# Optimization experiments

Hardware: AMD Instinct MI355X
Metric: run time of the kernel (lower is better)

## Reference

```python
import jax, jax.numpy as jnp
import numpy as np

EPS = 1e-6
BETA = 0.5
B, T, N = 128, 30, 10000   # batch, BP iterations, n error bits
M, K = 5000, 10            # checks, observables
CHK_W, OBS_W = 6, 50       # row weights of chkmat / obsmat


def _make_supports():
    """Deterministic sparse supports (CSR-style flattened col indices + row ids)."""
    rng = np.random.default_rng(0)
    chk_rows = np.argpartition(rng.random((M, N)), CHK_W, axis=1)[:, :CHK_W]
    obs_rows = np.argpartition(rng.random((K, N)), OBS_W, axis=1)[:, :OBS_W]
    chk_idx = chk_rows.reshape(-1).astype(np.int32)
    chk_seg = np.repeat(np.arange(M, dtype=np.int32), CHK_W)
    obs_idx = obs_rows.reshape(-1).astype(np.int32)
    obs_seg = np.repeat(np.arange(K, dtype=np.int32), OBS_W)
    return chk_idx, chk_seg, obs_idx, obs_seg


def setup_inputs() -> dict:
    key = jax.random.key(0)
    k1, k2, k3 = jax.random.split(key, 3)
    all_llrs = jax.random.normal(k1, (B, T, N), dtype=jnp.float32) * 2.0
    syndromes = jax.random.randint(k2, (B, M), 0, 2, dtype=jnp.int32)
    observables = jax.random.randint(k3, (B, K), 0, 2, dtype=jnp.int32)
    chk_idx, chk_seg, obs_idx, obs_seg = _make_supports()
    return {
        "all_llrs": all_llrs,
        "syndromes": syndromes,
        "observables": observables,
        "chk_idx": jnp.asarray(chk_idx),
        "chk_seg": jnp.asarray(chk_seg),
        "obs_idx": jnp.asarray(obs_idx),
        "obs_seg": jnp.asarray(obs_seg),
    }


def _pred_llr(t, idx, seg, num_seg):
    # t: (B,T,N) tanh(llr/2); gather support cols -> (B,T,E)
    g = t[:, :, idx]
    # segmented product over support entries (tanh rule), segments on axis 0
    p = jax.ops.segment_prod(jnp.moveaxis(g, 2, 0), seg, num_segments=num_seg)  # (S,B,T)
    p = jnp.clip(jnp.moveaxis(p, 0, 2), -1.0 + EPS, 1.0 - EPS)  # (B,T,S)
    return 2.0 * jnp.arctanh(p)


def _bce_with_logits(z, y):
    # stable BCEWithLogits: max(z,0) - z*y + log(1+exp(-|z|)) == logaddexp(0,z) - z*y
    return jnp.logaddexp(0.0, z) - z * y


def reference(all_llrs, syndromes, observables, chk_idx, chk_seg, obs_idx, obs_seg):
    t = jnp.tanh(all_llrs * 0.5)                                   # (B,T,N)
    syn_llr = _pred_llr(t, chk_idx, chk_seg, syndromes.shape[1])    # (B,T,M)
    obs_llr = _pred_llr(t, obs_idx, obs_seg, observables.shape[1])  # (B,T,K)
    y_syn = syndromes.astype(jnp.float32)[:, None, :]
    y_obs = observables.astype(jnp.float32)[:, None, :]
    loss1 = _bce_with_logits(-syn_llr, y_syn).sum(axis=2)           # (B,T)
    loss2 = _bce_with_logits(-obs_llr, y_obs).sum(axis=2)           # (B,T)
    loss = BETA * loss1 + (1.0 - BETA) * loss2
    return loss.mean()
```

## Files before the change

### kernel.cpp

```cpp
#include <hip/hip_runtime.h>
#include <hip/hip_bf16.h>

#define B_  128
#define T_  30
#define N_  10000
#define M_  5000
#define K_  10
#define CHK_W_ 6
#define OBS_W_ 50
#define EPS_ 1e-6f
#define LOG2_ 0.69314718056f

__global__ __launch_bounds__(256) void decode_loss_kernel(
    const float* __restrict__ all_llrs,
    const int*   __restrict__ syndromes,
    const int*   __restrict__ observables,
    const int*   __restrict__ chk_idx,
    const int*   __restrict__ obs_idx,
    float*       __restrict__ out)
{
    __shared__ float tn[N_];
    __shared__ float red[4];

    const int bt  = blockIdx.x;
    const int b   = bt / T_;
    const int tid = threadIdx.x;

    const float4* row4 = (const float4*)(all_llrs + (size_t)bt * N_);
    float4* tn4 = (float4*)tn;
    for (int i = tid; i < N_/4; i += 256) {
        float4 v = row4[i];
        float4 r;
        r.x = 1.f - 2.f / (__expf(v.x) + 1.f);
        r.y = 1.f - 2.f / (__expf(v.y) + 1.f);
        r.z = 1.f - 2.f / (__expf(v.z) + 1.f);
        r.w = 1.f - 2.f / (__expf(v.w) + 1.f);
        tn4[i] = r;
    }
    __syncthreads();

    float acc1 = 0.f;
    const int* syn = syndromes + (size_t)b * M_;
    for (int m = tid; m < M_; m += 256) {
        const int* ci = chk_idx + m * CHK_W_;
        float p = tn[ci[0]] * tn[ci[1]] * tn[ci[2]]
                * tn[ci[3]] * tn[ci[4]] * tn[ci[5]];
        p = fminf(fmaxf(p, -1.f + EPS_), 1.f - EPS_);
        float sp = syn[m] ? -p : p;
        acc1 += LOG2_ - __logf(1.f + sp);
    }

    float acc2 = 0.f;
    const int* obs = observables + (size_t)b * K_;
    for (int k = tid; k < K_; k += 256) {
        const int* oi = obs_idx + k * OBS_W_;
        float p = 1.f;
        #pragma unroll 10
        for (int j = 0; j < OBS_W_; ++j) p *= tn[oi[j]];
        p = fminf(fmaxf(p, -1.f + EPS_), 1.f - EPS_);
        float sp = obs[k] ? -p : p;
        acc2 += LOG2_ - __logf(1.f + sp);
    }

    float acc = 0.5f * acc1 + 0.5f * acc2;

    #pragma unroll
    for (int off = 32; off > 0; off >>= 1)
        acc += __shfl_down(acc, off, 64);
    if ((tid & 63) == 0) red[tid >> 6] = acc;
    __syncthreads();
    if (tid == 0) {
        float s = red[0] + red[1] + red[2] + red[3];
        atomicAdd(out, s * (1.f / (B_ * T_)));
    }
}

extern "C" void kernel_launch(void* const* d_in, const int* in_sizes, int n_in,
                              void* d_out, int out_size, void* d_ws, size_t ws_size,
                              hipStream_t stream) {
    const float* all_llrs    = (const float*)d_in[0];
    const int*   syndromes   = (const int*)d_in[1];
    const int*   observables = (const int*)d_in[2];
    const int*   chk_idx     = (const int*)d_in[3];
    const int*   obs_idx     = (const int*)d_in[5];
    float* out = (float*)d_out;

    hipMemsetAsync(out, 0, sizeof(float) * out_size, stream);

    dim3 grid(B_ * T_);
    dim3 block(256);
    decode_loss_kernel<<<grid, block, 0, stream>>>(
        all_llrs, syndromes, observables, chk_idx, obs_idx, out);
}
```

Baseline: 287.2 us.

## Split into tanh-transpose to fp16 column-major, then coalesced gather-loss kernel

A first kernel computes tanh and writes the result transposed to an (N, B*T) half-precision workspace. A second kernel has each lane handle two (b,t) rows as a half2 and gathers check and observable columns with coalesced loads, splitting checks into chunks across a 2D grid. This replaces the per-row LDS staging and scattered shared-memory gathers, but adds an extra pass through global memory and lowers the product to fp16 precision. Products of 50 fp16 terms may lose accuracy or underflow.

```diff
diff --git a/kernel.cpp b/kernel.cpp
--- a/kernel.cpp
+++ b/kernel.cpp
@@ -1,5 +1,5 @@
 #include <hip/hip_runtime.h>
-#include <hip/hip_bf16.h>
+#include <hip/hip_fp16.h>
 
 #define B_  128
 #define T_  30
@@ -9,69 +9,117 @@
 #define CHK_W_ 6
 #define OBS_W_ 50
 #define EPS_ 1e-6f
-#define LOG2_ 0.69314718056f
+#define LOG2F_ 0.69314718056f
+#define BT_ (B_*T_)
+#define RG_ 128
+#define NGRP_ (BT_/RG_)
+#define CHUNK_ 100
+#define NCHK_BLK_ (M_/CHUNK_)
 
-__global__ __launch_bounds__(256) void decode_loss_kernel(
-    const float* __restrict__ all_llrs,
-    const int*   __restrict__ syndromes,
-    const int*   __restrict__ observables,
-    const int*   __restrict__ chk_idx,
-    const int*   __restrict__ obs_idx,
-    float*       __restrict__ out)
+__global__ __launch_bounds__(256) void tanh_transpose_kernel(
+    const float* __restrict__ llrs,
+    __half*      __restrict__ tt)
 {
-    __shared__ float tn[N_];
-    __shared__ float red[4];
+    __shared__ float tile[64][65];
+    const int bt0 = blockIdx.x * 64;
+    const int n0  = blockIdx.y * 64;
+    const int tid = threadIdx.x;
+    const int c   = tid & 63;
+    const int r4  = tid >> 6;
 
-    const int bt  = blockIdx.x;
-    const int b   = bt / T_;
-    const int tid = threadIdx.x;
-
-    const float4* row4 = (const float4*)(all_llrs + (size_t)bt * N_);
-    float4* tn4 = (float4*)tn;
-    for (int i = tid; i < N_/4; i += 256) {
-        float4 v = row4[i];
-        float4 r;
-        r.x = 1.f - 2.f / (__expf(v.x) + 1.f);
-        r.y = 1.f - 2.f / (__expf(v.y) + 1.f);
-        r.z = 1.f - 2.f / (__expf(v.z) + 1.f);
-        r.w = 1.f - 2.f / (__expf(v.w) + 1.f);
-        tn4[i] = r;
+    if (n0 + c < N_) {
+        #pragma unroll
+        for (int i = 0; i < 16; ++i) {
+            int r = i * 4 + r4;
+            float v = llrs[(size_t)(bt0 + r) * N_ + (n0 + c)];
+            tile[r][c] = 1.f - 2.f / (__expf(v) + 1.f);
+        }
     }
     __syncthreads();
 
-    float acc1 = 0.f;
-    const int* syn = syndromes + (size_t)b * M_;
-    for (int m = tid; m < M_; m += 256) {
-        const int* ci = chk_idx + m * CHK_W_;
-        float p = tn[ci[0]] * tn[ci[1]] * tn[ci[2]]
-                * tn[ci[3]] * tn[ci[4]] * tn[ci[5]];
-        p = fminf(fmaxf(p, -1.f + EPS_), 1.f - EPS_);
-        float sp = syn[m] ? -p : p;
-        acc1 += LOG2_ - __logf(1.f + sp);
+    const int r = tid & 63;
+    #pragma unroll
+    for (int i = 0; i < 16; ++i) {
+        int cc = i * 4 + r4;
+        if (n0 + cc < N_)
+            tt[(size_t)(n0 + cc) * BT_ + (bt0 + r)] = __float2half(tile[r][cc]);
+    }
+}
+
+__global__ __launch_bounds__(256) void gather_loss_kernel(
+    const __half* __restrict__ tt,
+    const int*    __restrict__ syndromes,
+    const int*    __restrict__ observables,
+    const int*    __restrict__ chk_idx,
+    const int*    __restrict__ obs_idx,
+    float*        __restrict__ out)
+{
+    const int tid  = threadIdx.x;
+    const int lane = tid & 63;
+    const int wave = tid >> 6;
+    const int bt0  = blockIdx.x * RG_;
+    const int r0   = bt0 + 2 * lane;
+    const int b0   = r0 / T_;
+    const int b1   = (r0 + 1) / T_;
+    const __half2* tt2 = (const __half2*)tt;
+    const int half_off = r0 >> 1;
+
+    float acc = 0.f;
+    const int y = blockIdx.y;
+
+    if (y < NCHK_BLK_) {
+        const int* syn0 = syndromes + (size_t)b0 * M_;
+        const int* syn1 = syndromes + (size_t)b1 * M_;
+        const int m0 = y * CHUNK_ + wave * (CHUNK_ / 4);
+        #pragma unroll 2
+        for (int m = m0; m < m0 + CHUNK_ / 4; ++m) {
+            const int* ci = chk_idx + m * CHK_W_;
+            __half2 a0 = tt2[(size_t)ci[0] * (BT_/2) + half_off];
+            __half2 a1 = tt2[(size_t)ci[1] * (BT_/2) + half_off];
+            __half2 a2 = tt2[(size_t)ci[2] * (BT_/2) + half_off];
+            __half2 a3 = tt2[(size_t)ci[3] * (BT_/2) + half_off];
+            __half2 a4 = tt2[(size_t)ci[4] * (BT_/2) + half_off];
+            __half2 a5 = tt2[(size_t)ci[5] * (BT_/2) + half_off];
+            __half2 q  = __hmul2(__hmul2(__hmul2(a0, a1), __hmul2(a2, a3)),
+                                 __hmul2(a4, a5));
+            float p0 = __low2float(q);
+            float p1 = __high2float(q);
+            p0 = fminf(fmaxf(p0, -1.f + EPS_), 1.f - EPS_);
+            p1 = fminf(fmaxf(p1, -1.f + EPS_), 1.f - EPS_);
+            float sp0 = syn0[m] ? -p0 : p0;
+            float sp1 = syn1[m] ? -p1 : p1;
+            acc += (LOG2F_ - __logf(1.f + sp0))
+                 + (LOG2F_ - __logf(1.f + sp1));
+        }
+    } else {
+        const int* ob0 = observables + (size_t)b0 * K_;
+        const int* ob1 = observables + (size_t)b1 * K_;
+        for (int k = wave; k < K_; k += 4) {
+            const int* oi = obs_idx + k * OBS_W_;
+            __half2 q = __float2half2_rn(1.f);
+            #pragma unroll 10
+            for (int j = 0; j < OBS_W_; ++j)
+                q = __hmul2(q, tt2[(size_t)oi[j] * (BT_/2) + half_off]);
+            float p0 = __low2float(q);
+            float p1 = __high2float(q);
+            p0 = fminf(fmaxf(p0, -1.f + EPS_), 1.f - EPS_);
+            p1 = fminf(fmaxf(p1, -1.f + EPS_), 1.f - EPS_);
+            float sp0 = ob0[k] ? -p0 : p0;
+            float sp1 = ob1[k] ? -p1 : p1;
+            acc += (LOG2F_ - __logf(1.f + sp0))
+                 + (LOG2F_ - __logf(1.f + sp1));
+        }
     }
 
-    float acc2 = 0.f;
-    const int* obs = observables + (size_t)b * K_;
-    for (int k = tid; k < K_; k += 256) {
-        const int* oi = obs_idx + k * OBS_W_;
-        float p = 1.f;
-        #pragma unroll 10
-        for (int j = 0; j < OBS_W_; ++j) p *= tn[oi[j]];
-        p = fminf(fmaxf(p, -1.f + EPS_), 1.f - EPS_);
-        float sp = obs[k] ? -p : p;
-        acc2 += LOG2_ - __logf(1.f + sp);
-    }
-
-    float acc = 0.5f * acc1 + 0.5f * acc2;
-
+    __shared__ float red[4];
     #pragma unroll
     for (int off = 32; off > 0; off >>= 1)
         acc += __shfl_down(acc, off, 64);
-    if ((tid & 63) == 0) red[tid >> 6] = acc;
+    if (lane == 0) red[wave] = acc;
     __syncthreads();
     if (tid == 0) {
         float s = red[0] + red[1] + red[2] + red[3];
-        atomicAdd(out, s * (1.f / (B_ * T_)));
+        atomicAdd(out, s * (0.5f / BT_));
     }
 }
 
@@ -83,12 +131,15 @@
     const int*   observables = (const int*)d_in[2];
     const int*   chk_idx     = (const int*)d_in[3];
     const int*   obs_idx     = (const int*)d_in[5];
-    float* out = (float*)d_out;
+    float*  out = (float*)d_out;
+    __half* tt  = (__half*)d_ws;
 
     hipMemsetAsync(out, 0, sizeof(float) * out_size, stream);
 
-    dim3 grid(B_ * T_);
-    dim3 block(256);
-    decode_loss_kernel<<<grid, block, 0, stream>>>(
-        all_llrs, syndromes, observables, chk_idx, obs_idx, out);
+    dim3 g1(BT_ / 64, (N_ + 63) / 64);
+    tanh_transpose_kernel<<<g1, 256, 0, stream>>>(all_llrs, tt);
+
+    dim3 g2(NGRP_, NCHK_BLK_ + 1);
+    gather_loss_kernel<<<g2, 256, 0, stream>>>(
+        tt, syndromes, observables, chk_idx, obs_idx, out);
 }
```

After: 288.7 us. About the same (+0.5%).
